# Kernel tuning notes

Measured on AMD Instinct MI355X. Metric: run time of the kernel, lower is better.

## Reference

```python
import jax, jax.numpy as jnp
import numpy as np

B, T, U = 32, 4096, 512

def setup_inputs() -> dict:
    key = jax.random.key(0)
    k1, k2 = jax.random.split(key)
    x = jax.random.normal(k1, (B, T, U), dtype=jnp.float32)
    # learned per-channel smoothing coefficient (Keras 'uniform' init)
    b = jax.random.uniform(k2, (U,), dtype=jnp.float32)
    return {"x": x, "b": b}

def reference(x, b):
    # EMA recurrence: y_t = b * x_t + (1 - b) * y_{t-1}, y_0 state = 0.
    # First-order linear recurrence y_t = a * y_{t-1} + c_t solved with a
    # parallel (log-depth) associative scan over the time axis.
    a = 1.0 - b                      # (U,) decay per channel
    c = b * x                        # (B, T, U) input injection
    A = jnp.broadcast_to(a, c.shape) # (B, T, U)

    def combine(left, right):
        a_l, c_l = left
        a_r, c_r = right
        return (a_l * a_r, a_r * c_l + c_r)

    _, y = jax.lax.associative_scan(combine, (A, c), axis=1)
    return y  # (B, T, U) full output sequence
```

## Files before the change

kernel.cpp:

```cpp
#include <hip/hip_runtime.h>


namespace {

typedef float f4 __attribute__((ext_vector_type(4)));

constexpr int kB  = 32;
constexpr int kT  = 4096;
constexpr int kU4 = 512 / 4;
constexpr int kC  = 64;
constexpr int kL  = kT / kC;

constexpr size_t kWsNeed = (size_t)kB * kC * kU4 * sizeof(f4);

__device__ __forceinline__ f4 fma4(f4 a, f4 b, f4 c) {
  f4 r;
  r.x = fmaf(a.x, b.x, c.x);
  r.y = fmaf(a.y, b.y, c.y);
  r.z = fmaf(a.z, b.z, c.z);
  r.w = fmaf(a.w, b.w, c.w);
  return r;
}

__global__ __launch_bounds__(256) void ema_p1(
    const float* __restrict__ x, const float* __restrict__ bc,
    f4* __restrict__ S) {
  const int bid  = blockIdx.x;
  const int b    = bid >> 5;
  const int pair = bid & 31;
  const int sub  = threadIdx.x >> 7;
  const int u4   = threadIdx.x & 127;
  const int k    = pair * 2 + sub;

  const f4 bb = ((const f4*)bc)[u4];
  const f4 a  = 1.0f - bb;

  const f4* xp = (const f4*)x + ((size_t)b * kT + (size_t)k * kL) * kU4 + u4;
  f4 s = (f4)0.f;
  #pragma unroll 8
  for (int t = 0; t < kL; ++t) s = fma4(a, s, bb * xp[(size_t)t * kU4]);
  S[((size_t)b * kC + k) * kU4 + u4] = s;
}

__global__ __launch_bounds__(256) void ema_p23(
    const float* __restrict__ x, const float* __restrict__ bc,
    const f4* __restrict__ S, float* __restrict__ out) {
  const int bid  = blockIdx.x;
  const int b    = bid >> 5;
  const int pair = bid & 31;
  const int sub  = threadIdx.x >> 7;
  const int u4   = threadIdx.x & 127;
  const int k    = pair * 2 + sub;

  const f4 bb = ((const f4*)bc)[u4];
  const f4 a  = 1.0f - bb;
  f4 a64 = a;
  #pragma unroll
  for (int j = 0; j < 6; ++j) a64 *= a64;

  f4 e = (f4)0.f;
  f4 w = (f4)1.f;
  const f4* Sp = S + (size_t)b * kC * kU4 + u4;
  #pragma unroll 4
  for (int j = k - 1; j >= 0; --j) {
    e = fma4(w, Sp[(size_t)j * kU4], e);
    w *= a64;
  }

  const size_t off = ((size_t)b * kT + (size_t)k * kL) * kU4 + u4;
  const f4* xp = (const f4*)x + off;
  f4*       op = (f4*)out + off;
  f4 y = e;
  #pragma unroll 8
  for (int t = 0; t < kL; ++t) {
    y = fma4(a, y, bb * xp[(size_t)t * kU4]);
    __builtin_nontemporal_store(y, op + (size_t)t * kU4);
  }
}

__global__ __launch_bounds__(256) void ema_fallback(
    const float* __restrict__ x, const float* __restrict__ bc,
    float* __restrict__ out) {
  int g = blockIdx.x * 256 + threadIdx.x;
  if (g >= kB * kU4) return;
  int u4 = g % kU4;
  int b  = g / kU4;
  const f4 bb = ((const f4*)bc)[u4];
  const f4 a  = 1.0f - bb;
  f4 y = (f4)0.f;
  size_t off = (size_t)b * kT * kU4 + u4;
  const f4* xp = (const f4*)x + off;
  f4*       op = (f4*)out + off;
  for (int t = 0; t < kT; ++t) {
    y = fma4(a, y, bb * xp[(size_t)t * kU4]);
    op[(size_t)t * kU4] = y;
  }
}

}

extern "C" void kernel_launch(void* const* d_in, const int* in_sizes, int n_in,
                              void* d_out, int out_size, void* d_ws, size_t ws_size,
                              hipStream_t stream) {
  const float* x  = (const float*)d_in[0];
  const float* bc = (const float*)d_in[1];
  float* out = (float*)d_out;

  if (ws_size >= kWsNeed) {
    f4* S = (f4*)d_ws;
    const int grid = kB * (kC / 2);
    ema_p1 <<<grid, 256, 0, stream>>>(x, bc, S);
    ema_p23<<<grid, 256, 0, stream>>>(x, bc, S, out);
  } else {
    ema_fallback<<<(kB * kU4 + 255) / 256, 256, 0, stream>>>(x, bc, out);
  }
}
```

Measured before the change: 139.9 us.

## Stash chunk-local scan in fp16 workspace to avoid re-reading x

Pass 1 now writes each chunk's local scan result to the workspace as packed fp16, and pass 2 rebuilds the output as local + a^t * carry instead of re-reading x in fp32. This swaps a 256MB fp32 re-read for a 128MB fp16 write plus a 128MB fp16 read, so total traffic grows unless the stash stays in cache. Using fp16 for the intermediate adds precision loss, and the path needs a workspace of roughly 128MB or it falls back to the old two-pass code.

```diff
diff --git a/kernel.cpp b/kernel.cpp
--- a/kernel.cpp
+++ b/kernel.cpp
@@ -1,4 +1,5 @@
 #include <hip/hip_runtime.h>
+#include <hip/hip_fp16.h>
 
 
 namespace {
@@ -11,7 +12,10 @@
 constexpr int kC  = 64;
 constexpr int kL  = kT / kC;
 
-constexpr size_t kWsNeed = (size_t)kB * kC * kU4 * sizeof(f4);
+constexpr size_t kSBytes  = (size_t)kB * kC * kU4 * sizeof(f4);
+constexpr size_t kYlBytes = (size_t)kB * kT * kU4 * 8;
+constexpr size_t kWsNeedStash = kSBytes + kYlBytes;
+constexpr size_t kWsNeedBasic = kSBytes;
 
 __device__ __forceinline__ f4 fma4(f4 a, f4 b, f4 c) {
   f4 r;
@@ -22,29 +26,42 @@
   return r;
 }
 
-__global__ __launch_bounds__(256) void ema_p1(
-    const float* __restrict__ x, const float* __restrict__ bc,
-    f4* __restrict__ S) {
-  const int bid  = blockIdx.x;
-  const int b    = bid >> 5;
-  const int pair = bid & 31;
-  const int sub  = threadIdx.x >> 7;
-  const int u4   = threadIdx.x & 127;
-  const int k    = pair * 2 + sub;
-
-  const f4 bb = ((const f4*)bc)[u4];
-  const f4 a  = 1.0f - bb;
-
-  const f4* xp = (const f4*)x + ((size_t)b * kT + (size_t)k * kL) * kU4 + u4;
+union PkH4 { uint2 u; __half2 h[2]; };
+
+
+__global__ __launch_bounds__(256) void ema_s1(
+    const float* __restrict__ x, const float* __restrict__ bc,
+    f4* __restrict__ S, uint2* __restrict__ yl) {
+  const int bid  = blockIdx.x;
+  const int b    = bid >> 5;
+  const int pair = bid & 31;
+  const int sub  = threadIdx.x >> 7;
+  const int u4   = threadIdx.x & 127;
+  const int k    = pair * 2 + sub;
+
+  const f4 bb = ((const f4*)bc)[u4];
+  const f4 a  = 1.0f - bb;
+
+  const size_t off = ((size_t)b * kT + (size_t)k * kL) * kU4 + u4;
+  const f4* xp = (const f4*)x + off;
+  uint2*    yp = yl + off;
+
   f4 s = (f4)0.f;
   #pragma unroll 8
-  for (int t = 0; t < kL; ++t) s = fma4(a, s, bb * xp[(size_t)t * kU4]);
+  for (int t = 0; t < kL; ++t) {
+    f4 v = __builtin_nontemporal_load(xp + (size_t)t * kU4);
+    s = fma4(a, s, bb * v);
+    PkH4 pk;
+    pk.h[0] = __floats2half2_rn(s.x, s.y);
+    pk.h[1] = __floats2half2_rn(s.z, s.w);
+    yp[(size_t)t * kU4] = pk.u;
+  }
   S[((size_t)b * kC + k) * kU4 + u4] = s;
 }
 
-__global__ __launch_bounds__(256) void ema_p23(
-    const float* __restrict__ x, const float* __restrict__ bc,
-    const f4* __restrict__ S, float* __restrict__ out) {
+__global__ __launch_bounds__(256) void ema_s2(
+    const float* __restrict__ bc, const f4* __restrict__ S,
+    const uint2* __restrict__ yl, float* __restrict__ out) {
   const int bid  = blockIdx.x;
   const int b    = bid >> 5;
   const int pair = bid & 31;
@@ -68,6 +85,72 @@
   }
 
   const size_t off = ((size_t)b * kT + (size_t)k * kL) * kU4 + u4;
+  const uint2* yp = yl + off;
+  f4*          op = (f4*)out + off;
+  f4 p = a;
+  #pragma unroll 8
+  for (int t = 0; t < kL; ++t) {
+    PkH4 pk;
+    pk.u = yp[(size_t)t * kU4];
+    float2 lo = __half22float2(pk.h[0]);
+    float2 hi = __half22float2(pk.h[1]);
+    f4 yv;
+    yv.x = fmaf(p.x, e.x, lo.x);
+    yv.y = fmaf(p.y, e.y, lo.y);
+    yv.z = fmaf(p.z, e.z, hi.x);
+    yv.w = fmaf(p.w, e.w, hi.y);
+    __builtin_nontemporal_store(yv, op + (size_t)t * kU4);
+    p *= a;
+  }
+}
+
+
+__global__ __launch_bounds__(256) void ema_p1(
+    const float* __restrict__ x, const float* __restrict__ bc,
+    f4* __restrict__ S) {
+  const int bid  = blockIdx.x;
+  const int b    = bid >> 5;
+  const int pair = bid & 31;
+  const int sub  = threadIdx.x >> 7;
+  const int u4   = threadIdx.x & 127;
+  const int k    = pair * 2 + sub;
+
+  const f4 bb = ((const f4*)bc)[u4];
+  const f4 a  = 1.0f - bb;
+
+  const f4* xp = (const f4*)x + ((size_t)b * kT + (size_t)k * kL) * kU4 + u4;
+  f4 s = (f4)0.f;
+  #pragma unroll 8
+  for (int t = 0; t < kL; ++t) s = fma4(a, s, bb * xp[(size_t)t * kU4]);
+  S[((size_t)b * kC + k) * kU4 + u4] = s;
+}
+
+__global__ __launch_bounds__(256) void ema_p23(
+    const float* __restrict__ x, const float* __restrict__ bc,
+    const f4* __restrict__ S, float* __restrict__ out) {
+  const int bid  = blockIdx.x;
+  const int b    = bid >> 5;
+  const int pair = bid & 31;
+  const int sub  = threadIdx.x >> 7;
+  const int u4   = threadIdx.x & 127;
+  const int k    = pair * 2 + sub;
+
+  const f4 bb = ((const f4*)bc)[u4];
+  const f4 a  = 1.0f - bb;
+  f4 a64 = a;
+  #pragma unroll
+  for (int j = 0; j < 6; ++j) a64 *= a64;
+
+  f4 e = (f4)0.f;
+  f4 w = (f4)1.f;
+  const f4* Sp = S + (size_t)b * kC * kU4 + u4;
+  #pragma unroll 4
+  for (int j = k - 1; j >= 0; --j) {
+    e = fma4(w, Sp[(size_t)j * kU4], e);
+    w *= a64;
+  }
+
+  const size_t off = ((size_t)b * kT + (size_t)k * kL) * kU4 + u4;
   const f4* xp = (const f4*)x + off;
   f4*       op = (f4*)out + off;
   f4 y = e;
@@ -77,6 +160,7 @@
     __builtin_nontemporal_store(y, op + (size_t)t * kU4);
   }
 }
+
 
 __global__ __launch_bounds__(256) void ema_fallback(
     const float* __restrict__ x, const float* __restrict__ bc,
@@ -105,10 +189,15 @@
   const float* x  = (const float*)d_in[0];
   const float* bc = (const float*)d_in[1];
   float* out = (float*)d_out;
-
-  if (ws_size >= kWsNeed) {
+  const int grid = kB * (kC / 2);
+
+  if (ws_size >= kWsNeedStash) {
+    f4*    S  = (f4*)d_ws;
+    uint2* yl = (uint2*)((char*)d_ws + kSBytes);
+    ema_s1<<<grid, 256, 0, stream>>>(x, bc, S, yl);
+    ema_s2<<<grid, 256, 0, stream>>>(bc, S, yl, out);
+  } else if (ws_size >= kWsNeedBasic) {
     f4* S = (f4*)d_ws;
-    const int grid = kB * (kC / 2);
     ema_p1 <<<grid, 256, 0, stream>>>(x, bc, S);
     ema_p23<<<grid, 256, 0, stream>>>(x, bc, S, out);
   } else {
```

New measurement: 136.8 us. 1.02x faster.
